# Kernel tuning notes

Hardware: AMD Instinct MI355X
Metric: run time of the kernel (lower is better)

The kernel has to match this reference:

```python
import jax, jax.numpy as jnp
import numpy as np

B, N, DIM, H, DH, K = 4, 2048, 512, 6, 64, 16
KEEP_PROB = 0.9  # 1 - dropout_rate
LOG2PI = float(np.log(2.0 * np.pi))
LOG_PRIOR = float(np.log(1.0 / K))


def setup_inputs() -> dict:
    key = jax.random.key(0)
    ks = jax.random.split(key, 7)
    inputs_q = jax.random.normal(ks[0], (B, N, DIM), dtype=jnp.float32)
    # decoder-style causal mask, shape [B, 1, q_len, kv_len]
    causal = jnp.tril(jnp.ones((N, N), dtype=jnp.float32))
    mask = jnp.broadcast_to(causal[None, None], (B, 1, N, N))
    # dropout keep mask broadcast across the query dim: [B, H, 1, kv_len]
    keep = jax.random.bernoulli(ks[1], KEEP_PROB, (B, H, 1, N)).astype(jnp.float32)
    w_qkv = jax.random.normal(ks[2], (DIM, 3 * H * DH), dtype=jnp.float32) * 0.02
    w_out = jax.random.normal(ks[3], (H * DH, DIM), dtype=jnp.float32) * 0.02
    mu_lookup = jax.random.normal(ks[4], (K, DIM), dtype=jnp.float32)
    logvar_lookup = jax.random.normal(ks[5], (K, DIM), dtype=jnp.float32) * 0.1
    return {
        "inputs_q": inputs_q,
        "mask": mask,
        "keep": keep,
        "w_qkv": w_qkv,
        "w_out": w_out,
        "mu_lookup": mu_lookup,
        "logvar_lookup": logvar_lookup,
    }


def reference(inputs_q, mask, keep, w_qkv, w_out, mu_lookup, logvar_lookup):
    # --- MultiHeadDotProductAttention (self-attn path) ---
    qkv = (inputs_q @ w_qkv).reshape(B, N, 3, H, DH)  # [B,N,3,H,DH]
    q, k, v = qkv[:, :, 0], qkv[:, :, 1], qkv[:, :, 2]
    # bias: 0 where mask > 0, -1e10 elsewhere (note: no 1/sqrt(d) scaling, as in source)
    bias = jnp.where(mask > 0, 0.0, -1e10)
    attn_weights = jnp.einsum('bqhd,bkhd->bhqk', q, k) + bias  # [B,H,N,N]
    attn_weights = jax.nn.softmax(attn_weights, axis=-1)
    # broadcast dropout: mask shared across the query dim
    attn_weights = attn_weights * keep / KEEP_PROB
    attn_out = jnp.einsum('bhqk,bkhd->bqhd', attn_weights, v)
    attn_out = attn_out.reshape(B, N, H * DH) @ w_out  # [B,N,DIM]

    # --- GMM posterior approx q(y|x) ~= p(y|z) (approx_qy_x, vectorized over k) ---
    z = attn_out.mean(axis=1)  # pooled latent, [B,DIM]
    diff = z[:, None, :] - mu_lookup[None]  # [B,K,DIM]
    llh = -0.5 * jnp.sum(
        diff * diff / jnp.exp(logvar_lookup)[None] + logvar_lookup[None] + LOG2PI,
        axis=-1,
    )  # [B,K]
    logLogit_qy_x = llh + LOG_PRIOR
    qy_x = jax.nn.softmax(logLogit_qy_x, axis=1)  # [B,K]

    # combine mixture mean back in so both branches are live in one output
    return attn_out + (qy_x @ mu_lookup)[:, None, :]
```

## Files before the change

kernel.cpp:

```cpp
#include <hip/hip_runtime.h>
#include <cstdint>
#include <cstddef>

#define NH 6
#define NSEQ 2048
#define DIMD 512
#define BATCH 4
#define HD 384
#define LOG2PI_F 1.8378770664093453f
#define LOG2E_F 1.4426950408889634f
#define M12L2_F (-17.312340490667562f)

typedef __attribute__((ext_vector_type(8))) short short8;
typedef __attribute__((ext_vector_type(8))) unsigned short ushort8;
typedef __attribute__((ext_vector_type(4))) unsigned short ushort4v;
typedef __attribute__((ext_vector_type(4))) float floatx4;

__device__ inline unsigned short f2bf(float f){
  unsigned int u = __float_as_uint(f);
  u += 0x7FFFu + ((u>>16)&1u);
  return (unsigned short)(u>>16);
}

#define GLD16(gp, lp) __builtin_amdgcn_global_load_lds( \
  (const __attribute__((address_space(1))) void*)(gp), \
  (__attribute__((address_space(3))) void*)(lp), 16, 0, 0)

__device__ inline void wtrans_body(
    const float* __restrict__ src, unsigned short* __restrict__ dst,
    int R, int C, int bx, int by, unsigned short* Ls, int t)
{
  const int r = t>>2, c0 = (t&3)*16;
  const int d0 = by*64, n0 = bx*64;
  #pragma unroll
  for (int j=0;j<16;j+=4){
    floatx4 v = *(const floatx4*)(src + (size_t)(d0+r)*C + n0 + c0 + j);
    #pragma unroll
    for(int jj=0;jj<4;jj++) Ls[r*72 + c0+j+jj] = f2bf(v[jj]);
  }
  __syncthreads();
  #pragma unroll
  for (int j=0;j<16;j+=8){
    ushort8 o;
    #pragma unroll
    for(int jj=0;jj<8;jj++) o[jj] = Ls[(c0+j+jj)*72 + r];
    *(ushort8*)(dst + (size_t)(n0+r)*R + d0 + c0 + j) = o;
  }
}

__global__ __launch_bounds__(256) void prep(
    const float* __restrict__ xq, unsigned short* __restrict__ xbf,
    const float* __restrict__ w_qkv, unsigned short* __restrict__ wqT,
    const float* __restrict__ w_out, unsigned short* __restrict__ woT)
{
  __shared__ __attribute__((aligned(16))) unsigned short Ls[64*72];
  const int bid = blockIdx.x, t = threadIdx.x;
  if (bid < 4096){
    int i = bid*256 + t;
    floatx4 v = *(const floatx4*)(xq + (size_t)i*4);
    ushort4v r;
    #pragma unroll
    for(int j=0;j<4;j++) r[j] = f2bf(v[j]);
    *(ushort4v*)(xbf + (size_t)i*4) = r;
  } else if (bid < 4240){
    int rb = bid - 4096;
    wtrans_body(w_qkv, wqT, 512, 1152, rb%18, rb/18, Ls, t);
  } else {
    int rb = bid - 4240;
    wtrans_body(w_out, woT, 384, 512, rb%8, rb/8, Ls, t);
  }
}

__global__ __launch_bounds__(256) void gemm_qkv(
    const unsigned short* __restrict__ A,
    const unsigned short* __restrict__ Bt,
    const float* __restrict__ keep,
    unsigned short* __restrict__ Qo, unsigned short* __restrict__ Ko,
    unsigned short* __restrict__ Vt)
{
  __shared__ __attribute__((aligned(16))) unsigned short Cs[128*132];
  unsigned short* As = Cs;
  unsigned short* Bs = Cs + 128*64;
  const int tid = threadIdx.x;
  const int w = tid>>6, lane = tid&63;
  const int wr = w>>1, wc = w&1;
  const int quad = lane>>4, l16 = lane&15;
  const int tM = blockIdx.x*128, tN = blockIdx.y*128;
  const int r8 = lane>>3, c8 = (lane&7)*8;
  floatx4 acc[4][4];
  floatx4 zed = {0.f,0.f,0.f,0.f};
  #pragma unroll
  for (int i=0;i<4;i++)
    #pragma unroll
    for(int j=0;j<4;j++) acc[i][j] = zed;

  for (int k0=0; k0<512; k0+=64){
    #pragma unroll
    for (int i=0;i<4;i++){
      int row = w*32 + i*8;
      GLD16(A  + (size_t)(tM+row+r8)*512 + k0 + c8, As + row*64);
      GLD16(Bt + (size_t)(tN+row+r8)*512 + k0 + c8, Bs + row*64);
    }
    __syncthreads();
    #pragma unroll
    for (int kk=0; kk<64; kk+=32){
      short8 af[4], bf[4];
      #pragma unroll
      for(int mt=0;mt<4;mt++)
        af[mt] = *(const short8*)(As + (wr*64+mt*16+l16)*64 + kk + quad*8);
      #pragma unroll
      for(int nt=0;nt<4;nt++)
        bf[nt] = *(const short8*)(Bs + (wc*64+nt*16+l16)*64 + kk + quad*8);
      #pragma unroll
      for(int mt=0;mt<4;mt++)
        #pragma unroll
        for(int nt=0;nt<4;nt++)
          acc[mt][nt] = __builtin_amdgcn_mfma_f32_16x16x32_bf16(af[mt], bf[nt], acc[mt][nt], 0,0,0);
    }
    __syncthreads();
  }
  #pragma unroll
  for(int mt=0;mt<4;mt++)
    #pragma unroll
    for(int nt=0;nt<4;nt++){
      int gcol = tN + wc*64 + nt*16 + l16;
      float qs = (gcol < 384) ? LOG2E_F : 1.0f;
      #pragma unroll
      for(int r=0;r<4;r++)
        Cs[(wr*64+mt*16+quad*4+r)*132 + wc*64+nt*16+l16] = f2bf(acc[mt][nt][r]*qs);
    }
  __syncthreads();
  if (blockIdx.y < 6){
    const int row = tid>>1, colh = (tid&1)*64;
    const int gcol0 = tN + colh;
    const int t = gcol0/384, rem = gcol0 - t*384, h = rem>>6;
    const int grow = tM + row, b = grow>>11, n = grow & 2047;
    unsigned short* dst = (t==0 ? Qo : Ko) + ((size_t)((b*NH+h)*NSEQ+n))*64;
    #pragma unroll
    for(int j=0;j<8;j++)
      *(ushort8*)(dst + j*8) = *(const ushort8*)(Cs + row*132 + colh + j*8);
  } else {
    const int dcol = tid>>1;
    const int nh   = (tid&1)*64;
    const int gcol = tN + dcol;
    const int rem = gcol - 768, h = rem>>6, dh = rem&63;
    const int b = tM>>11, nb = tM & 2047;
    const float* kp = keep + (size_t)(b*NH+h)*NSEQ + nb + nh;
    unsigned short* dst = Vt + ((size_t)((b*NH+h)*64 + dh))*NSEQ + nb + nh;
    #pragma unroll
    for (int j8=0;j8<8;j8++){
      floatx4 k0 = *(const floatx4*)(kp + j8*8);
      floatx4 k1 = *(const floatx4*)(kp + j8*8 + 4);
      ushort8 o;
      #pragma unroll
      for(int u=0;u<4;u++)
        o[u]   = (k0[u] < 0.5f) ? (unsigned short)0 : Cs[(nh + j8*8 + u)*132 + dcol];
      #pragma unroll
      for(int u=0;u<4;u++)
        o[4+u] = (k1[u] < 0.5f) ? (unsigned short)0 : Cs[(nh + j8*8 + 4 + u)*132 + dcol];
      *(ushort8*)(dst + j8*8) = o;
    }
  }
}

__global__ __launch_bounds__(256, 3) void attn_kernel(
    const unsigned short* __restrict__ Qg, const unsigned short* __restrict__ Kg,
    const unsigned short* __restrict__ VtG,
    unsigned short* __restrict__ atp)
{
  __shared__ __attribute__((aligned(16))) char sm[4*32*68*4 + 4*32*4];
  const int tid = threadIdx.x;
  const int w = tid>>6, lane = tid&63;
  float* Oc   = (float*)sm;
  float* accs = (float*)(sm + 4*32*68*4);
  const int quad = lane>>4, l16 = lane&15;
  const int bid = blockIdx.x;
  const int idx = bid>>3;
  const int bh  = (bid&7) + 8*(idx % 3);
  const int c   = 63 - idx/3;
  const int b = bh/NH, h = bh - b*NH;
  const unsigned short* Qb = Qg  + (size_t)bh*NSEQ*64;
  const int q0 = c*32;
  const int nkt = (c>>1) + 1;
  const int q_abs0 = q0 + l16;

  const unsigned short* Kl = Kg  + (size_t)bh*NSEQ*64 + (size_t)l16*64 + quad*8;
  const unsigned short* Vl = VtG + (size_t)bh*64*NSEQ + (size_t)l16*NSEQ + quad*8;

  short8 qf[2][2];
  #pragma unroll
  for(int mt=0;mt<2;mt++)
    #pragma unroll
    for(int kc=0;kc<2;kc++)
      qf[mt][kc] = *(const short8*)(Qb + (size_t)(q0+mt*16+l16)*64 + kc*32 + quad*8);

  floatx4 O[2][4];
  float accl[2] = {0.f, 0.f};
  floatx4 zed = {0.f,0.f,0.f,0.f};
  floatx4 m12v = {M12L2_F, M12L2_F, M12L2_F, M12L2_F};
  #pragma unroll
  for(int mt=0;mt<2;mt++)
    #pragma unroll
    for(int dt=0;dt<4;dt++) O[mt][dt] = zed;

  for (int kt = w; kt < nkt; kt += 4){
    const int kB = kt*64;
    short8 vf[2][4];
    const unsigned short* vp0 = Vl + kB;
    #pragma unroll
    for(int kh=0;kh<2;kh++)
      #pragma unroll
      for(int dt=0;dt<4;dt++)
        vf[kh][dt] = *(const short8*)(vp0 + (size_t)dt*32768 + kh*32);

    floatx4 sacc[2][4];
    #pragma unroll
    for(int mt=0;mt<2;mt++)
      #pragma unroll
      for(int nt=0;nt<4;nt++) sacc[mt][nt] = m12v;
    const unsigned short* kp0 = Kl + (size_t)kt*4096;
    #pragma unroll
    for(int nt=0;nt<4;nt++){
      short8 kf0 = *(const short8*)(kp0 + nt*1024);
      short8 kf1 = *(const short8*)(kp0 + nt*1024 + 32);
      #pragma unroll
      for(int mt=0;mt<2;mt++){
        sacc[mt][nt] = __builtin_amdgcn_mfma_f32_16x16x32_bf16(kf0, qf[mt][0], sacc[mt][nt], 0,0,0);
        sacc[mt][nt] = __builtin_amdgcn_mfma_f32_16x16x32_bf16(kf1, qf[mt][1], sacc[mt][nt], 0,0,0);
      }
    }

    const bool dia = (kt == nkt-1);
    #pragma unroll
    for(int mt=0;mt<2;mt++){
      const int qa = q_abs0 + mt*16;
      unsigned int d0[4], d1[4];
      float rs = 0.f;
      #pragma unroll
      for(int nt=0;nt<4;nt++){
        const int key0 = kB + nt*16 + quad*4;
        float p0 = exp2f(sacc[mt][nt][0]);
        float p1 = exp2f(sacc[mt][nt][1]);
        float p2 = exp2f(sacc[mt][nt][2]);
        float p3 = exp2f(sacc[mt][nt][3]);
        if (dia){
          p0 = (key0   <= qa) ? p0 : 0.f;
          p1 = (key0+1 <= qa) ? p1 : 0.f;
          p2 = (key0+2 <= qa) ? p2 : 0.f;
          p3 = (key0+3 <= qa) ? p3 : 0.f;
        }
        rs += (p0+p1) + (p2+p3);
        asm("v_cvt_pk_bf16_f32 %0, %1, %2" : "=v"(d0[nt]) : "v"(p0), "v"(p1));
        asm("v_cvt_pk_bf16_f32 %0, %1, %2" : "=v"(d1[nt]) : "v"(p2), "v"(p3));
      }
      accl[mt] += rs;
      #pragma unroll
      for(int kh=0;kh<2;kh++){
        unsigned int x0 = d0[2*kh],   x1 = d1[2*kh];
        unsigned int y0 = d0[2*kh+1], y1 = d1[2*kh+1];
        asm("v_permlane32_swap_b32 %0, %1" : "+v"(x0), "+v"(y0));
        asm("v_permlane16_swap_b32 %0, %1" : "+v"(x0), "+v"(y0));
        asm("v_permlane32_swap_b32 %0, %1" : "+v"(x1), "+v"(y1));
        asm("v_permlane16_swap_b32 %0, %1" : "+v"(x1), "+v"(y1));
        union { unsigned int u[4]; short8 s; } cvt;
        cvt.u[0] = x0; cvt.u[1] = x1; cvt.u[2] = y0; cvt.u[3] = y1;
        short8 pf = cvt.s;
        #pragma unroll
        for(int dt=0;dt<4;dt++)
          O[mt][dt] = __builtin_amdgcn_mfma_f32_16x16x32_bf16(pf, vf[kh][dt], O[mt][dt], 0,0,0);
      }
    }
  }

  #pragma unroll
  for(int mt=0;mt<2;mt++){
    accl[mt] += __shfl_xor(accl[mt], 16, 64);
    accl[mt] += __shfl_xor(accl[mt], 32, 64);
  }

  {
    float* Ow = Oc + w*(32*68);
    #pragma unroll
    for(int mt=0;mt<2;mt++){
      #pragma unroll
      for(int dt=0;dt<4;dt++)
        #pragma unroll
        for(int r=0;r<4;r++)
          Ow[(mt*16+quad*4+r)*68 + dt*16 + l16] = O[mt][dt][r];
      if (quad == 0)
        accs[w*32 + mt*16 + l16] = accl[mt];
    }
  }
  __syncthreads();

  const int orow = tid>>3, oc0 = (tid&7)*8;
  float as = accs[0*32+orow] + accs[1*32+orow] + accs[2*32+orow] + accs[3*32+orow];
  float sc2 = (1.0f/0.9f) / as;
  float vsum[8];
  #pragma unroll
  for(int j=0;j<8;j++) vsum[j] = 0.f;
  #pragma unroll
  for(int s=0;s<4;s++){
    const float* p = Oc + s*(32*68) + orow*68 + oc0;
    #pragma unroll
    for(int j=0;j<8;j++) vsum[j] += p[j];
  }
  ushort8 o;
  #pragma unroll
  for(int j=0;j<8;j++) o[j] = f2bf(vsum[j]*sc2);
  unsigned short* dstp = atp + ((size_t)(b*NSEQ + q0 + orow))*HD + h*64 + oc0;
  *(ushort8*)dstp = o;
}

__global__ __launch_bounds__(256) void gemm_proj(
    const unsigned short* __restrict__ A,
    const unsigned short* __restrict__ Bt,
    float* __restrict__ out,
    float* __restrict__ z)
{
  __shared__ __attribute__((aligned(16))) unsigned short As[128*64];
  __shared__ __attribute__((aligned(16))) unsigned short Bs[128*64];
  const int tid = threadIdx.x;
  const int w = tid>>6, lane = tid&63;
  const int wr = w>>1, wc = w&1;
  const int quad = lane>>4, l16 = lane&15;
  const int tM = blockIdx.x*128, tN = blockIdx.y*128;
  const int r8 = lane>>3, c8 = (lane&7)*8;
  floatx4 acc[4][4];
  floatx4 zed = {0.f,0.f,0.f,0.f};
  #pragma unroll
  for (int i=0;i<4;i++)
    #pragma unroll
    for(int j=0;j<4;j++) acc[i][j] = zed;

  for (int k0=0; k0<384; k0+=64){
    #pragma unroll
    for (int i=0;i<4;i++){
      int row = w*32 + i*8;
      GLD16(A  + (size_t)(tM+row+r8)*384 + k0 + c8, As + row*64);
      GLD16(Bt + (size_t)(tN+row+r8)*384 + k0 + c8, Bs + row*64);
    }
    __syncthreads();
    #pragma unroll
    for (int kk=0; kk<64; kk+=32){
      short8 af[4], bf[4];
      #pragma unroll
      for(int mt=0;mt<4;mt++)
        af[mt] = *(const short8*)(As + (wr*64+mt*16+l16)*64 + kk + quad*8);
      #pragma unroll
      for(int nt=0;nt<4;nt++)
        bf[nt] = *(const short8*)(Bs + (wc*64+nt*16+l16)*64 + kk + quad*8);
      #pragma unroll
      for(int mt=0;mt<4;mt++)
        #pragma unroll
        for(int nt=0;nt<4;nt++)
          acc[mt][nt] = __builtin_amdgcn_mfma_f32_16x16x32_bf16(af[mt], bf[nt], acc[mt][nt], 0,0,0);
    }
    __syncthreads();
  }
  #pragma unroll
  for(int mt=0;mt<4;mt++){
    int grow = tM + wr*64 + mt*16 + quad*4;
    #pragma unroll
    for(int nt=0;nt<4;nt++){
      int gcol = tN + wc*64 + nt*16 + l16;
      #pragma unroll
      for(int r=0;r<4;r++)
        out[(size_t)(grow+r)*512 + gcol] = acc[mt][nt][r];
    }
  }
  #pragma unroll
  for(int nt=0;nt<4;nt++){
    float s = 0.f;
    #pragma unroll
    for(int mt=0;mt<4;mt++)
      #pragma unroll
      for(int r=0;r<4;r++) s += acc[mt][nt][r];
    s += __shfl_xor(s, 16, 64);
    s += __shfl_xor(s, 32, 64);
    if (quad == 0){
      int gcol = tN + wc*64 + nt*16 + l16;
      atomicAdd(&z[(tM>>11)*DIMD + gcol], s);
    }
  }
}

__global__ __launch_bounds__(256) void gmm_kernel(
    const float* __restrict__ z, const float* __restrict__ mu,
    const float* __restrict__ lv, float* __restrict__ c)
{
  __shared__ float sh[16];
  __shared__ float qy[16];
  int tid = threadIdx.x;
  int k = tid>>4, li = tid&15;
  int b = blockIdx.x;
  float part = 0.f;
  for(int d=li; d<DIMD; d+=16){
    float zz = z[b*DIMD+d] * (1.0f/2048.0f);
    float m = mu[k*DIMD+d], l = lv[k*DIMD+d];
    float diff = zz - m;
    part += diff*diff*__expf(-l) + l + LOG2PI_F;
  }
  #pragma unroll
  for(int off=8;off>=1;off>>=1) part += __shfl_xor(part, off, 64);
  if (li==0) sh[k] = part;
  __syncthreads();
  if (tid<16){
    float logit = -0.5f*sh[tid];
    float mx = logit;
    #pragma unroll
    for(int off=8;off>=1;off>>=1) mx = fmaxf(mx, __shfl_xor(mx, off, 64));
    float e = __expf(logit-mx);
    float se = e;
    #pragma unroll
    for(int off=8;off>=1;off>>=1) se += __shfl_xor(se, off, 64);
    qy[tid] = e/se;
  }
  __syncthreads();
  for(int d=tid; d<DIMD; d+=256){
    float accv = 0.f;
    #pragma unroll
    for(int kk=0;kk<16;kk++) accv += qy[kk]*mu[kk*DIMD+d];
    c[b*DIMD+d] = accv;
  }
}

__global__ __launch_bounds__(256) void final_add(
    float* __restrict__ out, const float* __restrict__ c)
{
  size_t i = ((size_t)blockIdx.x*256 + threadIdx.x)*4;
  int d = (int)(i & 511);
  int b = (int)(i >> 20);
  floatx4 a = *(const floatx4*)(out + i);
  floatx4 cc = *(const floatx4*)(c + b*DIMD + d);
  *(floatx4*)(out + i) = a + cc;
}

extern "C" void kernel_launch(void* const* d_in, const int* in_sizes, int n_in,
                              void* d_out, int out_size, void* d_ws, size_t ws_size,
                              hipStream_t stream) {
  const float* inputs_q = (const float*)d_in[0];
  const float* keep  = (const float*)d_in[2];
  const float* w_qkv = (const float*)d_in[3];
  const float* w_out = (const float*)d_in[4];
  const float* mu    = (const float*)d_in[5];
  const float* lv    = (const float*)d_in[6];
  float* out = (float*)d_out;
  char* ws = (char*)d_ws;
  size_t off = 0;
  auto alloc = [&](size_t bytes){ void* p = ws + off; off += (bytes + 255) & ~(size_t)255; return p; };
  unsigned short* Qb  = (unsigned short*)alloc((size_t)24*2048*64*2);
  unsigned short* Kb  = (unsigned short*)alloc((size_t)24*2048*64*2);
  unsigned short* Vt  = (unsigned short*)alloc((size_t)24*64*2048*2);
  unsigned short* xbf = (unsigned short*)alloc((size_t)8192*512*2);
  unsigned short* wqT = (unsigned short*)alloc((size_t)1152*512*2);
  unsigned short* woT = (unsigned short*)alloc((size_t)512*384*2);
  unsigned short* atp = (unsigned short*)alloc((size_t)8192*384*2);
  float* z  = (float*)alloc((size_t)4*512*4);
  float* c  = (float*)alloc((size_t)4*512*4);

  hipMemsetAsync(z, 0, 4*512*4, stream);
  prep<<<4288, 256, 0, stream>>>(inputs_q, xbf, w_qkv, wqT, w_out, woT);
  gemm_qkv<<<dim3(64,9), 256, 0, stream>>>(xbf, wqT, keep, Qb, Kb, Vt);
  attn_kernel<<<1536, 256, 0, stream>>>(Qb, Kb, Vt, atp);
  gemm_proj<<<dim3(64,4), 256, 0, stream>>>(atp, woT, out, z);
  gmm_kernel<<<4, 256, 0, stream>>>(z, mu, lv, c);
  final_add<<<4096, 256, 0, stream>>>(out, c);
}
```

Measured before the change: 234.9 us.

## Reorder pooled GMM before projection, fuse mixture-mean add into projection epilogue

The mean over sequence is taken on the attention output before the output projection: attention blocks atomically add per-head row sums, and the GMM kernel multiplies the pooled vector by w_out itself, so its bias vector is ready before the projection GEMM. The projection epilogue then adds the mixture mean directly, which removes the final_add pass over the output and the z atomics in the projection GEMM. The attention kernel also prefetches the next K tile into registers and uses the raw hardware exp2. Risks are extra atomics from every attention block, a serial 384-long fp32 matvec in a 4-block GMM kernel, and a slightly different rounding order (pooling bf16-rounded versus fp32 values).

```diff
diff --git a/kernel.cpp b/kernel.cpp
--- a/kernel.cpp
+++ b/kernel.cpp
@@ -20,6 +20,14 @@
   unsigned int u = __float_as_uint(f);
   u += 0x7FFFu + ((u>>16)&1u);
   return (unsigned short)(u>>16);
+}
+
+__device__ inline float exp2_raw(float x){
+#if __has_builtin(__builtin_amdgcn_exp2f)
+  return __builtin_amdgcn_exp2f(x);
+#else
+  float r; asm("v_exp_f32 %0, %1" : "=v"(r) : "v"(x)); return r;
+#endif
 }
 
 #define GLD16(gp, lp) __builtin_amdgcn_global_load_lds( \
@@ -166,7 +174,8 @@
 __global__ __launch_bounds__(256, 3) void attn_kernel(
     const unsigned short* __restrict__ Qg, const unsigned short* __restrict__ Kg,
     const unsigned short* __restrict__ VtG,
-    unsigned short* __restrict__ atp)
+    unsigned short* __restrict__ atp,
+    float* __restrict__ zsum)
 {
   __shared__ __attribute__((aligned(16))) char sm[4*32*68*4 + 4*32*4];
   const int tid = threadIdx.x;
@@ -203,6 +212,16 @@
     #pragma unroll
     for(int dt=0;dt<4;dt++) O[mt][dt] = zed;
 
+  short8 kf[4][2];
+  {
+    const unsigned short* kp0 = Kl + (size_t)w*4096;
+    #pragma unroll
+    for(int nt=0;nt<4;nt++){
+      kf[nt][0] = *(const short8*)(kp0 + nt*1024);
+      kf[nt][1] = *(const short8*)(kp0 + nt*1024 + 32);
+    }
+  }
+
   for (int kt = w; kt < nkt; kt += 4){
     const int kB = kt*64;
     short8 vf[2][4];
@@ -218,15 +237,21 @@
     for(int mt=0;mt<2;mt++)
       #pragma unroll
       for(int nt=0;nt<4;nt++) sacc[mt][nt] = m12v;
-    const unsigned short* kp0 = Kl + (size_t)kt*4096;
-    #pragma unroll
-    for(int nt=0;nt<4;nt++){
-      short8 kf0 = *(const short8*)(kp0 + nt*1024);
-      short8 kf1 = *(const short8*)(kp0 + nt*1024 + 32);
+    #pragma unroll
+    for(int nt=0;nt<4;nt++)
       #pragma unroll
       for(int mt=0;mt<2;mt++){
-        sacc[mt][nt] = __builtin_amdgcn_mfma_f32_16x16x32_bf16(kf0, qf[mt][0], sacc[mt][nt], 0,0,0);
-        sacc[mt][nt] = __builtin_amdgcn_mfma_f32_16x16x32_bf16(kf1, qf[mt][1], sacc[mt][nt], 0,0,0);
+        sacc[mt][nt] = __builtin_amdgcn_mfma_f32_16x16x32_bf16(kf[nt][0], qf[mt][0], sacc[mt][nt], 0,0,0);
+        sacc[mt][nt] = __builtin_amdgcn_mfma_f32_16x16x32_bf16(kf[nt][1], qf[mt][1], sacc[mt][nt], 0,0,0);
+      }
+    __builtin_amdgcn_sched_barrier(0);
+    {
+      const int ktn = (kt+4 < nkt) ? kt+4 : kt;
+      const unsigned short* kpn = Kl + (size_t)ktn*4096;
+      #pragma unroll
+      for(int nt=0;nt<4;nt++){
+        kf[nt][0] = *(const short8*)(kpn + nt*1024);
+        kf[nt][1] = *(const short8*)(kpn + nt*1024 + 32);
       }
     }
 
@@ -239,10 +264,10 @@
       #pragma unroll
       for(int nt=0;nt<4;nt++){
         const int key0 = kB + nt*16 + quad*4;
-        float p0 = exp2f(sacc[mt][nt][0]);
-        float p1 = exp2f(sacc[mt][nt][1]);
-        float p2 = exp2f(sacc[mt][nt][2]);
-        float p3 = exp2f(sacc[mt][nt][3]);
+        float p0 = exp2_raw(sacc[mt][nt][0]);
+        float p1 = exp2_raw(sacc[mt][nt][1]);
+        float p2 = exp2_raw(sacc[mt][nt][2]);
+        float p3 = exp2_raw(sacc[mt][nt][3]);
         if (dia){
           p0 = (key0   <= qa) ? p0 : 0.f;
           p1 = (key0+1 <= qa) ? p1 : 0.f;
@@ -296,27 +321,91 @@
   const int orow = tid>>3, oc0 = (tid&7)*8;
   float as = accs[0*32+orow] + accs[1*32+orow] + accs[2*32+orow] + accs[3*32+orow];
   float sc2 = (1.0f/0.9f) / as;
-  float vsum[8];
-  #pragma unroll
-  for(int j=0;j<8;j++) vsum[j] = 0.f;
+  float fv[8];
+  #pragma unroll
+  for(int j=0;j<8;j++) fv[j] = 0.f;
   #pragma unroll
   for(int s=0;s<4;s++){
     const float* p = Oc + s*(32*68) + orow*68 + oc0;
     #pragma unroll
-    for(int j=0;j<8;j++) vsum[j] += p[j];
+    for(int j=0;j<8;j++) fv[j] += p[j];
   }
   ushort8 o;
   #pragma unroll
-  for(int j=0;j<8;j++) o[j] = f2bf(vsum[j]*sc2);
+  for(int j=0;j<8;j++){ fv[j] *= sc2; o[j] = f2bf(fv[j]); }
   unsigned short* dstp = atp + ((size_t)(b*NSEQ + q0 + orow))*HD + h*64 + oc0;
   *(ushort8*)dstp = o;
+
+  #pragma unroll
+  for(int j=0;j<8;j++){
+    fv[j] += __shfl_xor(fv[j], 8, 64);
+    fv[j] += __shfl_xor(fv[j], 16, 64);
+    fv[j] += __shfl_xor(fv[j], 32, 64);
+  }
+  if (lane < 8){
+    #pragma unroll
+    for(int j=0;j<8;j++)
+      atomicAdd(&zsum[(size_t)b*HD + h*64 + lane*8 + j], fv[j]);
+  }
+}
+
+__global__ __launch_bounds__(256) void gmm_kernel(
+    const float* __restrict__ zsum,
+    const float* __restrict__ wo,
+    const float* __restrict__ mu,
+    const float* __restrict__ lv, float* __restrict__ c)
+{
+  __shared__ float zsl[384];
+  __shared__ float zl[512];
+  __shared__ float sh[16];
+  __shared__ float qy[16];
+  const int tid = threadIdx.x, b = blockIdx.x;
+  for(int i=tid;i<384;i+=256) zsl[i] = zsum[(size_t)b*384+i];
+  __syncthreads();
+  #pragma unroll
+  for(int dd=0;dd<2;dd++){
+    const int d = tid + dd*256;
+    float s = 0.f;
+    for(int e=0;e<384;e++) s += zsl[e]*wo[(size_t)e*512+d];
+    zl[d] = s*(1.0f/2048.0f);
+  }
+  __syncthreads();
+  const int k = tid>>4, li = tid&15;
+  float part = 0.f;
+  for(int d=li; d<DIMD; d+=16){
+    float m = mu[k*DIMD+d], l = lv[k*DIMD+d];
+    float diff = zl[d] - m;
+    part += diff*diff*__expf(-l) + l + LOG2PI_F;
+  }
+  #pragma unroll
+  for(int off=8;off>=1;off>>=1) part += __shfl_xor(part, off, 64);
+  if (li==0) sh[k] = part;
+  __syncthreads();
+  if (tid<16){
+    float logit = -0.5f*sh[tid];
+    float mx = logit;
+    #pragma unroll
+    for(int off=8;off>=1;off>>=1) mx = fmaxf(mx, __shfl_xor(mx, off, 64));
+    float e = __expf(logit-mx);
+    float se = e;
+    #pragma unroll
+    for(int off=8;off>=1;off>>=1) se += __shfl_xor(se, off, 64);
+    qy[tid] = e/se;
+  }
+  __syncthreads();
+  for(int d=tid; d<DIMD; d+=256){
+    float accv = 0.f;
+    #pragma unroll
+    for(int kk=0;kk<16;kk++) accv += qy[kk]*mu[kk*DIMD+d];
+    c[b*DIMD+d] = accv;
+  }
 }
 
 __global__ __launch_bounds__(256) void gemm_proj(
     const unsigned short* __restrict__ A,
     const unsigned short* __restrict__ Bt,
-    float* __restrict__ out,
-    float* __restrict__ z)
+    const float* __restrict__ cvec,
+    float* __restrict__ out)
 {
   __shared__ __attribute__((aligned(16))) unsigned short As[128*64];
   __shared__ __attribute__((aligned(16))) unsigned short Bs[128*64];
@@ -358,82 +447,19 @@
     }
     __syncthreads();
   }
-  #pragma unroll
-  for(int mt=0;mt<4;mt++){
-    int grow = tM + wr*64 + mt*16 + quad*4;
-    #pragma unroll
-    for(int nt=0;nt<4;nt++){
-      int gcol = tN + wc*64 + nt*16 + l16;
+  const int bq = tM>>11;
+  #pragma unroll
+  for(int nt=0;nt<4;nt++){
+    const int gcol = tN + wc*64 + nt*16 + l16;
+    const float cc = cvec[bq*DIMD + gcol];
+    #pragma unroll
+    for(int mt=0;mt<4;mt++){
+      const int grow = tM + wr*64 + mt*16 + quad*4;
       #pragma unroll
       for(int r=0;r<4;r++)
-        out[(size_t)(grow+r)*512 + gcol] = acc[mt][nt][r];
-    }
-  }
-  #pragma unroll
-  for(int nt=0;nt<4;nt++){
-    float s = 0.f;
-    #pragma unroll
-    for(int mt=0;mt<4;mt++)
-      #pragma unroll
-      for(int r=0;r<4;r++) s += acc[mt][nt][r];
-    s += __shfl_xor(s, 16, 64);
-    s += __shfl_xor(s, 32, 64);
-    if (quad == 0){
-      int gcol = tN + wc*64 + nt*16 + l16;
-      atomicAdd(&z[(tM>>11)*DIMD + gcol], s);
-    }
-  }
-}
-
-__global__ __launch_bounds__(256) void gmm_kernel(
-    const float* __restrict__ z, const float* __restrict__ mu,
-    const float* __restrict__ lv, float* __restrict__ c)
-{
-  __shared__ float sh[16];
-  __shared__ float qy[16];
-  int tid = threadIdx.x;
-  int k = tid>>4, li = tid&15;
-  int b = blockIdx.x;
-  float part = 0.f;
-  for(int d=li; d<DIMD; d+=16){
-    float zz = z[b*DIMD+d] * (1.0f/2048.0f);
-    float m = mu[k*DIMD+d], l = lv[k*DIMD+d];
-    float diff = zz - m;
-    part += diff*diff*__expf(-l) + l + LOG2PI_F;
-  }
-  #pragma unroll
-  for(int off=8;off>=1;off>>=1) part += __shfl_xor(part, off, 64);
-  if (li==0) sh[k] = part;
-  __syncthreads();
-  if (tid<16){
-    float logit = -0.5f*sh[tid];
-    float mx = logit;
-    #pragma unroll
-    for(int off=8;off>=1;off>>=1) mx = fmaxf(mx, __shfl_xor(mx, off, 64));
-    float e = __expf(logit-mx);
-    float se = e;
-    #pragma unroll
-    for(int off=8;off>=1;off>>=1) se += __shfl_xor(se, off, 64);
-    qy[tid] = e/se;
-  }
-  __syncthreads();
-  for(int d=tid; d<DIMD; d+=256){
-    float accv = 0.f;
-    #pragma unroll
-    for(int kk=0;kk<16;kk++) accv += qy[kk]*mu[kk*DIMD+d];
-    c[b*DIMD+d] = accv;
-  }
-}
-
-__global__ __launch_bounds__(256) void final_add(
-    float* __restrict__ out, const float* __restrict__ c)
-{
-  size_t i = ((size_t)blockIdx.x*256 + threadIdx.x)*4;
-  int d = (int)(i & 511);
-  int b = (int)(i >> 20);
-  floatx4 a = *(const floatx4*)(out + i);
-  floatx4 cc = *(const floatx4*)(c + b*DIMD + d);
-  *(floatx4*)(out + i) = a + cc;
+        out[(size_t)(grow+r)*512 + gcol] = acc[mt][nt][r] + cc;
+    }
+  }
 }
 
 extern "C" void kernel_launch(void* const* d_in, const int* in_sizes, int n_in,
@@ -456,14 +482,13 @@
   unsigned short* wqT = (unsigned short*)alloc((size_t)1152*512*2);
   unsigned short* woT = (unsigned short*)alloc((size_t)512*384*2);
   unsigned short* atp = (unsigned short*)alloc((size_t)8192*384*2);
-  float* z  = (float*)alloc((size_t)4*512*4);
-  float* c  = (float*)alloc((size_t)4*512*4);
-
-  hipMemsetAsync(z, 0, 4*512*4, stream);
+  float* zsum = (float*)alloc((size_t)4*384*4);
+  float* c    = (float*)alloc((size_t)4*512*4);
+
+  hipMemsetAsync(zsum, 0, 4*384*4, stream);
   prep<<<4288, 256, 0, stream>>>(inputs_q, xbf, w_qkv, wqT, w_out, woT);
   gemm_qkv<<<dim3(64,9), 256, 0, stream>>>(xbf, wqT, keep, Qb, Kb, Vt);
-  attn_kernel<<<1536, 256, 0, stream>>>(Qb, Kb, Vt, atp);
-  gemm_proj<<<dim3(64,4), 256, 0, stream>>>(atp, woT, out, z);
-  gmm_kernel<<<4, 256, 0, stream>>>(z, mu, lv, c);
-  final_add<<<4096, 256, 0, stream>>>(out, c);
-}
+  attn_kernel<<<1536, 256, 0, stream>>>(Qb, Kb, Vt, atp, zsum);
+  gmm_kernel<<<4, 256, 0, stream>>>(zsum, w_out, mu, lv, c);
+  gemm_proj<<<dim3(64,4), 256, 0, stream>>>(atp, woT, c, out);
+}
```

Result: slower. 330.2 us (+40.6%).
